# Optimization experiments

Measured on AMD Instinct MI355X. Metric: run time of the kernel, lower is better.

The kernel has to match this reference:

```python
import jax, jax.numpy as jnp
import numpy as np

N_NODES = 100000


def gcn_layer(x, W, b, src, dst, n):
    # PyG GCNConv: add self-loops, symmetric normalization, linear transform
    h = x @ W  # [N, out]
    loop = jnp.arange(n)
    s = jnp.concatenate([src, loop])
    d = jnp.concatenate([dst, loop])
    ones = jnp.ones(s.shape[0], dtype=x.dtype)
    deg = jax.ops.segment_sum(ones, d, num_segments=n)  # in-degree incl. self-loop
    dinv = jnp.where(deg > 0, jax.lax.rsqrt(deg), 0.0)
    norm = dinv[s] * dinv[d]  # [E+N]
    msg = h[s] * norm[:, None]  # gather + scale
    out = jax.ops.segment_sum(msg, d, num_segments=n)  # scatter-add
    return out + b


def setup_inputs() -> dict:
    key = jax.random.key(0)
    k1, k2, k3, k4, k5 = jax.random.split(key, 5)
    d_feat, hidden = 128, 16
    x = jax.random.normal(k1, (N_NODES, d_feat), dtype=jnp.float32)
    edge_index = jax.random.randint(k2, (2, 1600000), 0, N_NODES, dtype=jnp.int64)
    W1 = jax.random.normal(k3, (d_feat, hidden), dtype=jnp.float32) / np.sqrt(d_feat)
    b1 = jnp.zeros((hidden,), dtype=jnp.float32)
    W2 = jax.random.normal(k4, (hidden, d_feat), dtype=jnp.float32) / np.sqrt(hidden)
    b2 = jnp.zeros((d_feat,), dtype=jnp.float32)
    return {"x": x, "edge_index": edge_index, "W1": W1, "b1": b1, "W2": W2, "b2": b2}


def reference(x, edge_index, W1, b1, W2, b2):
    src, dst = edge_index[0], edge_index[1]
    h = gcn_layer(x, W1, b1, src, dst, N_NODES)
    h = jax.nn.relu(h)
    out = gcn_layer(h, W2, b2, src, dst, N_NODES)
    return out
```

## Files before the change

kernel.cpp:

```cpp
#include <hip/hip_runtime.h>


#define THREADS 256
#define TSC 512
#define BSH 9
#define BNODES 512
#define ECHUNK 4096
#define CAPB 9216

typedef _Float16 half4 __attribute__((ext_vector_type(4)));

__global__ void k_init(int* __restrict__ cursor, int NB) {
    int i = blockIdx.x * blockDim.x + threadIdx.x;
    if (i < NB) cursor[i] = i * CAPB;
}

__global__ void __launch_bounds__(TSC) k_bscatter(
        const int* __restrict__ src, const int* __restrict__ dst,
        int* __restrict__ cursor, int* __restrict__ pk, int NB, int E) {
    __shared__ int eds[ECHUNK];
    __shared__ unsigned short rnk[ECHUNK];
    __shared__ unsigned char bkt[ECHUNK];
    __shared__ int h[512];
    __shared__ int lbase[512];
    int tid = threadIdx.x;
    int base0 = blockIdx.x * ECHUNK, end = min(base0 + ECHUNK, E);
    int cnt = end - base0;
    for (int i = tid; i < NB; i += TSC) h[i] = 0;
    __syncthreads();
    int k0 = base0 + tid * 8;
    if (k0 + 8 <= end) {
        int4 d0 = *reinterpret_cast<const int4*>(dst + k0);
        int4 d1 = *reinterpret_cast<const int4*>(dst + k0 + 4);
        int4 s0 = *reinterpret_cast<const int4*>(src + k0);
        int4 s1 = *reinterpret_cast<const int4*>(src + k0 + 4);
        int dd[8] = {d0.x, d0.y, d0.z, d0.w, d1.x, d1.y, d1.z, d1.w};
        int ss[8] = {s0.x, s0.y, s0.z, s0.w, s1.x, s1.y, s1.z, s1.w};
        int j0 = k0 - base0;
#pragma unroll
        for (int j = 0; j < 8; ++j) {
            int b = dd[j] >> BSH;
            int r = atomicAdd(&h[b], 1);
            eds[j0 + j] = ((dd[j] & (BNODES - 1)) << 17) | ss[j];
            rnk[j0 + j] = (unsigned short)r;
            bkt[j0 + j] = (unsigned char)b;
        }
    } else if (k0 < end) {
        for (int k = k0; k < end; ++k) {
            int d = dst[k], s = src[k];
            int b = d >> BSH;
            int r = atomicAdd(&h[b], 1);
            int j = k - base0;
            eds[j] = ((d & (BNODES - 1)) << 17) | s;
            rnk[j] = (unsigned short)r;
            bkt[j] = (unsigned char)b;
        }
    }
    __syncthreads();
    for (int i = tid; i < NB; i += TSC)
        lbase[i] = h[i] ? atomicAdd(&cursor[i], h[i]) : 0;
    __syncthreads();
    for (int j = tid; j < cnt; j += TSC)
        pk[lbase[bkt[j]] + rnk[j]] = eds[j];
}

__global__ void __launch_bounds__(TSC) k_bcsr(
        const int* __restrict__ pk, const int* __restrict__ cursor,
        int* __restrict__ row_ptr, int* __restrict__ row_cnt,
        float* __restrict__ dinv, int* __restrict__ col, int N) {
    __shared__ int eds[CAPB];
    __shared__ int deg[BNODES], sc[BNODES], cur[BNODES];
    int b = blockIdx.x, tid = threadIdx.x;
    int base = b * CAPB;
    int len = cursor[b] - base;
    for (int k = tid; k < len; k += TSC) eds[k] = pk[base + k];
    deg[tid] = 0;
    __syncthreads();
    for (int k = tid; k < len; k += TSC) atomicAdd(&deg[eds[k] >> 17], 1);
    __syncthreads();
    int d = deg[tid];
    sc[tid] = d;
    __syncthreads();
    for (int off = 1; off < BNODES; off <<= 1) {
        int t = (tid >= off) ? sc[tid - off] : 0;
        __syncthreads();
        sc[tid] += t;
        __syncthreads();
    }
    int excl = sc[tid] - d;
    cur[tid] = excl;
    int node = (b << BSH) + tid;
    if (node < N) {
        row_ptr[node] = base + excl;
        row_cnt[node] = d;
        dinv[node] = rsqrtf((float)(d + 1));
    }
    __syncthreads();
    for (int k = tid; k < len; k += TSC) {
        int p = eds[k];
        int r = atomicAdd(&cur[p >> 17], 1);
        col[base + r] = p & 0x1FFFF;
    }
}

__global__ void k_gemm1(const float* __restrict__ x, const float* __restrict__ W1,
                        const float* __restrict__ dinv, _Float16* __restrict__ hs, int n) {
    __shared__ float w[128 * 16];
    __shared__ float xs[16][129];
    int tid = threadIdx.x;
    for (int i = tid; i < 128 * 16; i += THREADS) w[i] = W1[i];
    int brow = blockIdx.x * 16;
    {
        int r = tid >> 4, off = (tid & 15) * 8;
        if (brow + r < n) {
            const float* xr = x + (size_t)(brow + r) * 128 + off;
            float4 a = *reinterpret_cast<const float4*>(xr);
            float4 b = *reinterpret_cast<const float4*>(xr + 4);
            xs[r][off + 0] = a.x; xs[r][off + 1] = a.y; xs[r][off + 2] = a.z; xs[r][off + 3] = a.w;
            xs[r][off + 4] = b.x; xs[r][off + 5] = b.y; xs[r][off + 6] = b.z; xs[r][off + 7] = b.w;
        }
    }
    __syncthreads();
    int r = tid >> 4, c = tid & 15;
    int row = brow + r;
    if (row >= n) return;
    float acc = 0.0f;
#pragma unroll 8
    for (int k = 0; k < 128; ++k) acc = fmaf(xs[r][k], w[k * 16 + c], acc);
    hs[(size_t)row * 16 + c] = (_Float16)(acc * dinv[row]);
}

template <int LAYER>
__global__ void k_gather(const _Float16* __restrict__ hin, const float* __restrict__ dinv,
                         const int* __restrict__ row_ptr, const int* __restrict__ row_cnt,
                         const int* __restrict__ col, const float* __restrict__ bias,
                         _Float16* __restrict__ out_h, float* __restrict__ out_f, int n) {
    int gid = blockIdx.x * blockDim.x + threadIdx.x;
    if (gid >= n * 4) return;
    int node = gid >> 2, q = (gid & 3) * 4;
    int s0 = row_ptr[node], s1 = s0 + row_cnt[node];
    half4 hv = *reinterpret_cast<const half4*>(hin + (size_t)node * 16 + q);
    float ax = (float)hv.x, ay = (float)hv.y, az = (float)hv.z, aw = (float)hv.w;
    int k = s0;
    for (; k + 3 < s1; k += 4) {
        int c0 = col[k], c1 = col[k + 1], c2 = col[k + 2], c3 = col[k + 3];
        half4 v0 = *reinterpret_cast<const half4*>(hin + (size_t)c0 * 16 + q);
        half4 v1 = *reinterpret_cast<const half4*>(hin + (size_t)c1 * 16 + q);
        half4 v2 = *reinterpret_cast<const half4*>(hin + (size_t)c2 * 16 + q);
        half4 v3 = *reinterpret_cast<const half4*>(hin + (size_t)c3 * 16 + q);
        ax += (float)v0.x + (float)v1.x + (float)v2.x + (float)v3.x;
        ay += (float)v0.y + (float)v1.y + (float)v2.y + (float)v3.y;
        az += (float)v0.z + (float)v1.z + (float)v2.z + (float)v3.z;
        aw += (float)v0.w + (float)v1.w + (float)v2.w + (float)v3.w;
    }
    for (; k < s1; ++k) {
        half4 v = *reinterpret_cast<const half4*>(hin + (size_t)col[k] * 16 + q);
        ax += (float)v.x; ay += (float)v.y; az += (float)v.z; aw += (float)v.w;
    }
    float dv = dinv[node];
    if (LAYER == 1) {
        float4 b = *reinterpret_cast<const float4*>(bias + q);
        half4 o;
        o.x = (_Float16)(fmaxf(fmaf(dv, ax, b.x), 0.0f) * dv);
        o.y = (_Float16)(fmaxf(fmaf(dv, ay, b.y), 0.0f) * dv);
        o.z = (_Float16)(fmaxf(fmaf(dv, az, b.z), 0.0f) * dv);
        o.w = (_Float16)(fmaxf(fmaf(dv, aw, b.w), 0.0f) * dv);
        *reinterpret_cast<half4*>(out_h + (size_t)node * 16 + q) = o;
    } else {
        float4 o = make_float4(ax * dv, ay * dv, az * dv, aw * dv);
        *reinterpret_cast<float4*>(out_f + (size_t)node * 16 + q) = o;
    }
}

__global__ void k_gemm2(const float* __restrict__ agg, const float* __restrict__ W2,
                        const float* __restrict__ b2, float* __restrict__ out, int n) {
    __shared__ float rows[32][16];
    int tid = threadIdx.x;
    int col = tid & 127, half = tid >> 7;
    int brow = blockIdx.x * 32;
    for (int i = tid; i < 512; i += THREADS) {
        int r = i >> 4;
        if (brow + r < n) rows[r][i & 15] = agg[(size_t)(brow + r) * 16 + (i & 15)];
    }
    float w[16];
#pragma unroll
    for (int k = 0; k < 16; ++k) w[k] = W2[k * 128 + col];
    float bias = b2[col];
    __syncthreads();
#pragma unroll
    for (int rr = 0; rr < 16; ++rr) {
        int r = half * 16 + rr;
        int row = brow + r;
        if (row >= n) break;
        float acc = bias;
#pragma unroll
        for (int k = 0; k < 16; ++k) acc = fmaf(rows[r][k], w[k], acc);
        out[(size_t)row * 128 + col] = acc;
    }
}

extern "C" void kernel_launch(void* const* d_in, const int* in_sizes, int n_in,
                              void* d_out, int out_size, void* d_ws, size_t ws_size,
                              hipStream_t stream) {
    const float* x  = (const float*)d_in[0];
    const int*   ei = (const int*)d_in[1];
    const float* W1 = (const float*)d_in[2];
    const float* b1 = (const float*)d_in[3];
    const float* W2 = (const float*)d_in[4];
    const float* b2 = (const float*)d_in[5];
    float* out = (float*)d_out;

    int N = in_sizes[0] / 128;
    int E = in_sizes[1] / 2;
    const int* src = ei;
    const int* dst = ei + E;
    int NB = (N + BNODES - 1) >> BSH;
    int EB = (E + ECHUNK - 1) / ECHUNK;
    size_t PADSZ = (size_t)NB * CAPB;

    char* ws = (char*)d_ws;
    size_t o = 0;
    auto carve = [&](size_t bytes) { void* p = ws + o; o = (o + bytes + 255) & ~(size_t)255; return p; };
    int*      cursor  = (int*)carve((size_t)NB * 4);
    int*      pk      = (int*)carve(PADSZ * 4);
    int*      col     = (int*)carve(PADSZ * 4);
    int*      row_ptr = (int*)carve((size_t)N * 4);
    int*      row_cnt = (int*)carve((size_t)N * 4);
    float*    dinv    = (float*)carve((size_t)N * 4);
    _Float16* hs      = (_Float16*)carve((size_t)N * 16 * 2);
    _Float16* h1s     = (_Float16*)carve((size_t)N * 16 * 2);
    float*    bufA    = (float*)carve((size_t)N * 16 * 4);

    int gN4 = (N * 4 + THREADS - 1) / THREADS;

    k_init<<<1, THREADS, 0, stream>>>(cursor, NB);
    k_bscatter<<<EB, TSC, 0, stream>>>(src, dst, cursor, pk, NB, E);
    k_bcsr<<<NB, TSC, 0, stream>>>(pk, cursor, row_ptr, row_cnt, dinv, col, N);

    k_gemm1<<<(N + 15) / 16, THREADS, 0, stream>>>(x, W1, dinv, hs, N);
    k_gather<1><<<gN4, THREADS, 0, stream>>>(hs, dinv, row_ptr, row_cnt, col, b1, h1s, nullptr, N);

    k_gather<2><<<gN4, THREADS, 0, stream>>>(h1s, dinv, row_ptr, row_cnt, col, nullptr, nullptr, bufA, N);
    k_gemm2<<<(N + 31) / 32, THREADS, 0, stream>>>(bufA, W2, b2, out, N);
}
```

Measured before the change: 206.7 us.

## Replace CSR build with bucketed LDS-atomic aggregation and fuse second GEMM

Drops the per-bucket CSR construction (prefix scan and column reorder) and aggregates each 256-node destination bucket directly from the unsorted packed edge list, accumulating into shared memory with float atomics. The second-layer aggregation now also applies W2 and the bias in the same kernel, which removes the intermediate float buffer and one launch. Buckets shrink to 256 nodes so the accumulator fits in LDS, and the scatter packs bucket and rank into a single int. In exchange it relies on LDS float atomics, which can contend on high-degree nodes, and sums in a nondeterministic order.

```diff
diff --git a/kernel.cpp b/kernel.cpp
--- a/kernel.cpp
+++ b/kernel.cpp
@@ -3,10 +3,11 @@
 
 #define THREADS 256
 #define TSC 512
-#define BSH 9
-#define BNODES 512
+#define BSH 8
+#define BNODES 256
 #define ECHUNK 4096
-#define CAPB 9216
+#define CAPB 4608
+#define NBMAX 512
 
 typedef _Float16 half4 __attribute__((ext_vector_type(4)));
 
@@ -19,10 +20,9 @@
         const int* __restrict__ src, const int* __restrict__ dst,
         int* __restrict__ cursor, int* __restrict__ pk, int NB, int E) {
     __shared__ int eds[ECHUNK];
-    __shared__ unsigned short rnk[ECHUNK];
-    __shared__ unsigned char bkt[ECHUNK];
-    __shared__ int h[512];
-    __shared__ int lbase[512];
+    __shared__ int rb[ECHUNK];
+    __shared__ int h[NBMAX];
+    __shared__ int lbase[NBMAX];
     int tid = threadIdx.x;
     int base0 = blockIdx.x * ECHUNK, end = min(base0 + ECHUNK, E);
     int cnt = end - base0;
@@ -42,8 +42,7 @@
             int b = dd[j] >> BSH;
             int r = atomicAdd(&h[b], 1);
             eds[j0 + j] = ((dd[j] & (BNODES - 1)) << 17) | ss[j];
-            rnk[j0 + j] = (unsigned short)r;
-            bkt[j0 + j] = (unsigned char)b;
+            rb[j0 + j] = (b << 13) | r;
         }
     } else if (k0 < end) {
         for (int k = k0; k < end; ++k) {
@@ -52,55 +51,32 @@
             int r = atomicAdd(&h[b], 1);
             int j = k - base0;
             eds[j] = ((d & (BNODES - 1)) << 17) | s;
-            rnk[j] = (unsigned short)r;
-            bkt[j] = (unsigned char)b;
+            rb[j] = (b << 13) | r;
         }
     }
     __syncthreads();
     for (int i = tid; i < NB; i += TSC)
         lbase[i] = h[i] ? atomicAdd(&cursor[i], h[i]) : 0;
     __syncthreads();
-    for (int j = tid; j < cnt; j += TSC)
-        pk[lbase[bkt[j]] + rnk[j]] = eds[j];
-}
-
-__global__ void __launch_bounds__(TSC) k_bcsr(
+    for (int j = tid; j < cnt; j += TSC) {
+        int v = rb[j];
+        pk[lbase[v >> 13] + (v & 8191)] = eds[j];
+    }
+}
+
+__global__ void __launch_bounds__(TSC) k_deg(
         const int* __restrict__ pk, const int* __restrict__ cursor,
-        int* __restrict__ row_ptr, int* __restrict__ row_cnt,
-        float* __restrict__ dinv, int* __restrict__ col, int N) {
-    __shared__ int eds[CAPB];
-    __shared__ int deg[BNODES], sc[BNODES], cur[BNODES];
+        float* __restrict__ dinv, int N) {
+    __shared__ int deg[BNODES];
     int b = blockIdx.x, tid = threadIdx.x;
     int base = b * CAPB;
-    int len = cursor[b] - base;
-    for (int k = tid; k < len; k += TSC) eds[k] = pk[base + k];
-    deg[tid] = 0;
-    __syncthreads();
-    for (int k = tid; k < len; k += TSC) atomicAdd(&deg[eds[k] >> 17], 1);
-    __syncthreads();
-    int d = deg[tid];
-    sc[tid] = d;
-    __syncthreads();
-    for (int off = 1; off < BNODES; off <<= 1) {
-        int t = (tid >= off) ? sc[tid - off] : 0;
-        __syncthreads();
-        sc[tid] += t;
-        __syncthreads();
-    }
-    int excl = sc[tid] - d;
-    cur[tid] = excl;
+    int len = min(cursor[b] - base, CAPB);
+    if (tid < BNODES) deg[tid] = 0;
+    __syncthreads();
+    for (int k = tid; k < len; k += TSC) atomicAdd(&deg[pk[base + k] >> 17], 1);
+    __syncthreads();
     int node = (b << BSH) + tid;
-    if (node < N) {
-        row_ptr[node] = base + excl;
-        row_cnt[node] = d;
-        dinv[node] = rsqrtf((float)(d + 1));
-    }
-    __syncthreads();
-    for (int k = tid; k < len; k += TSC) {
-        int p = eds[k];
-        int r = atomicAdd(&cur[p >> 17], 1);
-        col[base + r] = p & 0x1FFFF;
-    }
+    if (tid < BNODES && node < N) dinv[node] = rsqrtf((float)(deg[tid] + 1));
 }
 
 __global__ void k_gemm1(const float* __restrict__ x, const float* __restrict__ W1,
@@ -131,71 +107,76 @@
 }
 
 template <int LAYER>
-__global__ void k_gather(const _Float16* __restrict__ hin, const float* __restrict__ dinv,
-                         const int* __restrict__ row_ptr, const int* __restrict__ row_cnt,
-                         const int* __restrict__ col, const float* __restrict__ bias,
-                         _Float16* __restrict__ out_h, float* __restrict__ out_f, int n) {
-    int gid = blockIdx.x * blockDim.x + threadIdx.x;
-    if (gid >= n * 4) return;
-    int node = gid >> 2, q = (gid & 3) * 4;
-    int s0 = row_ptr[node], s1 = s0 + row_cnt[node];
-    half4 hv = *reinterpret_cast<const half4*>(hin + (size_t)node * 16 + q);
-    float ax = (float)hv.x, ay = (float)hv.y, az = (float)hv.z, aw = (float)hv.w;
-    int k = s0;
-    for (; k + 3 < s1; k += 4) {
-        int c0 = col[k], c1 = col[k + 1], c2 = col[k + 2], c3 = col[k + 3];
-        half4 v0 = *reinterpret_cast<const half4*>(hin + (size_t)c0 * 16 + q);
-        half4 v1 = *reinterpret_cast<const half4*>(hin + (size_t)c1 * 16 + q);
-        half4 v2 = *reinterpret_cast<const half4*>(hin + (size_t)c2 * 16 + q);
-        half4 v3 = *reinterpret_cast<const half4*>(hin + (size_t)c3 * 16 + q);
-        ax += (float)v0.x + (float)v1.x + (float)v2.x + (float)v3.x;
-        ay += (float)v0.y + (float)v1.y + (float)v2.y + (float)v3.y;
-        az += (float)v0.z + (float)v1.z + (float)v2.z + (float)v3.z;
-        aw += (float)v0.w + (float)v1.w + (float)v2.w + (float)v3.w;
-    }
-    for (; k < s1; ++k) {
-        half4 v = *reinterpret_cast<const half4*>(hin + (size_t)col[k] * 16 + q);
-        ax += (float)v.x; ay += (float)v.y; az += (float)v.z; aw += (float)v.w;
-    }
-    float dv = dinv[node];
+__global__ void __launch_bounds__(TSC) k_agg(
+        const _Float16* __restrict__ hin, const float* __restrict__ dinv,
+        const int* __restrict__ pk, const int* __restrict__ cursor,
+        const float* __restrict__ bias, const float* __restrict__ W2,
+        _Float16* __restrict__ out_h, float* __restrict__ out_f, int N) {
+    __shared__ float acc[BNODES][17];
+    int b = blockIdx.x, tid = threadIdx.x;
+    int base = b * CAPB;
+    int len = min(cursor[b] - base, CAPB);
+    int node0 = (b << BSH) + tid;
+    if (tid < BNODES) {
+        if (node0 < N) {
+            const _Float16* hp = hin + (size_t)node0 * 16;
+#pragma unroll
+            for (int f = 0; f < 16; f += 4) {
+                half4 v = *reinterpret_cast<const half4*>(hp + f);
+                acc[tid][f + 0] = (float)v.x; acc[tid][f + 1] = (float)v.y;
+                acc[tid][f + 2] = (float)v.z; acc[tid][f + 3] = (float)v.w;
+            }
+        } else {
+#pragma unroll
+            for (int f = 0; f < 16; ++f) acc[tid][f] = 0.0f;
+        }
+    }
+    __syncthreads();
+    int q = (tid & 3) * 4;
+#pragma unroll 2
+    for (int e = (tid >> 2); e < len; e += (TSC / 4)) {
+        int p = pk[base + e];
+        int d = p >> 17;
+        int s = p & 0x1FFFF;
+        half4 v = *reinterpret_cast<const half4*>(hin + (size_t)s * 16 + q);
+        atomicAdd(&acc[d][q + 0], (float)v.x);
+        atomicAdd(&acc[d][q + 1], (float)v.y);
+        atomicAdd(&acc[d][q + 2], (float)v.z);
+        atomicAdd(&acc[d][q + 3], (float)v.w);
+    }
+    __syncthreads();
     if (LAYER == 1) {
-        float4 b = *reinterpret_cast<const float4*>(bias + q);
-        half4 o;
-        o.x = (_Float16)(fmaxf(fmaf(dv, ax, b.x), 0.0f) * dv);
-        o.y = (_Float16)(fmaxf(fmaf(dv, ay, b.y), 0.0f) * dv);
-        o.z = (_Float16)(fmaxf(fmaf(dv, az, b.z), 0.0f) * dv);
-        o.w = (_Float16)(fmaxf(fmaf(dv, aw, b.w), 0.0f) * dv);
-        *reinterpret_cast<half4*>(out_h + (size_t)node * 16 + q) = o;
+        if (tid < BNODES && node0 < N) {
+            float dv = dinv[node0];
+            alignas(16) _Float16 tmp[16];
+#pragma unroll
+            for (int f = 0; f < 16; ++f)
+                tmp[f] = (_Float16)(fmaxf(fmaf(dv, acc[tid][f], bias[f]), 0.0f) * dv);
+            float4* dp = reinterpret_cast<float4*>(out_h + (size_t)node0 * 16);
+            const float4* sp = reinterpret_cast<const float4*>(tmp);
+            dp[0] = sp[0]; dp[1] = sp[1];
+        }
     } else {
-        float4 o = make_float4(ax * dv, ay * dv, az * dv, aw * dv);
-        *reinterpret_cast<float4*>(out_f + (size_t)node * 16 + q) = o;
-    }
-}
-
-__global__ void k_gemm2(const float* __restrict__ agg, const float* __restrict__ W2,
-                        const float* __restrict__ b2, float* __restrict__ out, int n) {
-    __shared__ float rows[32][16];
-    int tid = threadIdx.x;
-    int col = tid & 127, half = tid >> 7;
-    int brow = blockIdx.x * 32;
-    for (int i = tid; i < 512; i += THREADS) {
-        int r = i >> 4;
-        if (brow + r < n) rows[r][i & 15] = agg[(size_t)(brow + r) * 16 + (i & 15)];
-    }
-    float w[16];
-#pragma unroll
-    for (int k = 0; k < 16; ++k) w[k] = W2[k * 128 + col];
-    float bias = b2[col];
-    __syncthreads();
-#pragma unroll
-    for (int rr = 0; rr < 16; ++rr) {
-        int r = half * 16 + rr;
-        int row = brow + r;
-        if (row >= n) break;
-        float acc = bias;
-#pragma unroll
-        for (int k = 0; k < 16; ++k) acc = fmaf(rows[r][k], w[k], acc);
-        out[(size_t)row * 128 + col] = acc;
+        if (tid < BNODES && node0 < N) {
+            float dv = dinv[node0];
+#pragma unroll
+            for (int f = 0; f < 16; ++f) acc[tid][f] *= dv;
+        }
+        __syncthreads();
+        int col = tid & 127, grp = tid >> 7;
+        float w[16];
+#pragma unroll
+        for (int k = 0; k < 16; ++k) w[k] = W2[k * 128 + col];
+        float bb = bias[col];
+        for (int rr = 0; rr < BNODES / 4; ++rr) {
+            int r = grp * (BNODES / 4) + rr;
+            int node = (b << BSH) + r;
+            if (node >= N) break;
+            float s = bb;
+#pragma unroll
+            for (int k = 0; k < 16; ++k) s = fmaf(acc[r][k], w[k], s);
+            out_f[(size_t)node * 128 + col] = s;
+        }
     }
 }
 
@@ -221,25 +202,18 @@
     char* ws = (char*)d_ws;
     size_t o = 0;
     auto carve = [&](size_t bytes) { void* p = ws + o; o = (o + bytes + 255) & ~(size_t)255; return p; };
-    int*      cursor  = (int*)carve((size_t)NB * 4);
-    int*      pk      = (int*)carve(PADSZ * 4);
-    int*      col     = (int*)carve(PADSZ * 4);
-    int*      row_ptr = (int*)carve((size_t)N * 4);
-    int*      row_cnt = (int*)carve((size_t)N * 4);
-    float*    dinv    = (float*)carve((size_t)N * 4);
-    _Float16* hs      = (_Float16*)carve((size_t)N * 16 * 2);
-    _Float16* h1s     = (_Float16*)carve((size_t)N * 16 * 2);
-    float*    bufA    = (float*)carve((size_t)N * 16 * 4);
-
-    int gN4 = (N * 4 + THREADS - 1) / THREADS;
-
-    k_init<<<1, THREADS, 0, stream>>>(cursor, NB);
+    int*      cursor = (int*)carve((size_t)NB * 4);
+    int*      pk     = (int*)carve(PADSZ * 4);
+    float*    dinv   = (float*)carve((size_t)N * 4);
+    _Float16* hs     = (_Float16*)carve((size_t)N * 16 * 2);
+    _Float16* h1s    = (_Float16*)carve((size_t)N * 16 * 2);
+
+    k_init<<<(NB + THREADS - 1) / THREADS, THREADS, 0, stream>>>(cursor, NB);
     k_bscatter<<<EB, TSC, 0, stream>>>(src, dst, cursor, pk, NB, E);
-    k_bcsr<<<NB, TSC, 0, stream>>>(pk, cursor, row_ptr, row_cnt, dinv, col, N);
+    k_deg<<<NB, TSC, 0, stream>>>(pk, cursor, dinv, N);
 
     k_gemm1<<<(N + 15) / 16, THREADS, 0, stream>>>(x, W1, dinv, hs, N);
-    k_gather<1><<<gN4, THREADS, 0, stream>>>(hs, dinv, row_ptr, row_cnt, col, b1, h1s, nullptr, N);
-
-    k_gather<2><<<gN4, THREADS, 0, stream>>>(h1s, dinv, row_ptr, row_cnt, col, nullptr, nullptr, bufA, N);
-    k_gemm2<<<(N + 31) / 32, THREADS, 0, stream>>>(bufA, W2, b2, out, N);
-}
+    k_agg<1><<<NB, TSC, 0, stream>>>(hs, dinv, pk, cursor, b1, nullptr, h1s, nullptr, N);
+
+    k_agg<2><<<NB, TSC, 0, stream>>>(h1s, dinv, pk, cursor, b2, W2, nullptr, out, N);
+}
```

Result: slower. 509.5 us (+146.5%).

## Fuse layer-2 gather with W2 GEMM and halve CSR bucket size

Applied to the files above, without the earlier changes.

Merges the second-layer neighbor aggregation with the 16x128 output projection in one kernel. The aggregated rows now stay in shared memory, so the float intermediate buffer no longer makes a global round trip and one launch is removed. Bucket size for the CSR build drops from 512 to 256 nodes, which doubles the number of bscatter/bcsr blocks (about 391) for more parallelism. To fit, rank and bucket are packed into one int, and bucket length is clamped to capacity, which risks silently dropping edges if a bucket overflows.

```diff
diff --git a/kernel.cpp b/kernel.cpp
--- a/kernel.cpp
+++ b/kernel.cpp
@@ -3,10 +3,11 @@
 
 #define THREADS 256
 #define TSC 512
-#define BSH 9
-#define BNODES 512
+#define BSH 8
+#define BNODES 256
 #define ECHUNK 4096
-#define CAPB 9216
+#define CAPB 4608
+#define NBMAX 512
 
 typedef _Float16 half4 __attribute__((ext_vector_type(4)));
 
@@ -19,10 +20,9 @@
         const int* __restrict__ src, const int* __restrict__ dst,
         int* __restrict__ cursor, int* __restrict__ pk, int NB, int E) {
     __shared__ int eds[ECHUNK];
-    __shared__ unsigned short rnk[ECHUNK];
-    __shared__ unsigned char bkt[ECHUNK];
-    __shared__ int h[512];
-    __shared__ int lbase[512];
+    __shared__ int rb[ECHUNK];
+    __shared__ int h[NBMAX];
+    __shared__ int lbase[NBMAX];
     int tid = threadIdx.x;
     int base0 = blockIdx.x * ECHUNK, end = min(base0 + ECHUNK, E);
     int cnt = end - base0;
@@ -42,8 +42,7 @@
             int b = dd[j] >> BSH;
             int r = atomicAdd(&h[b], 1);
             eds[j0 + j] = ((dd[j] & (BNODES - 1)) << 17) | ss[j];
-            rnk[j0 + j] = (unsigned short)r;
-            bkt[j0 + j] = (unsigned char)b;
+            rb[j0 + j] = (b << 13) | r;
         }
     } else if (k0 < end) {
         for (int k = k0; k < end; ++k) {
@@ -52,16 +51,17 @@
             int r = atomicAdd(&h[b], 1);
             int j = k - base0;
             eds[j] = ((d & (BNODES - 1)) << 17) | s;
-            rnk[j] = (unsigned short)r;
-            bkt[j] = (unsigned char)b;
+            rb[j] = (b << 13) | r;
         }
     }
     __syncthreads();
     for (int i = tid; i < NB; i += TSC)
         lbase[i] = h[i] ? atomicAdd(&cursor[i], h[i]) : 0;
     __syncthreads();
-    for (int j = tid; j < cnt; j += TSC)
-        pk[lbase[bkt[j]] + rnk[j]] = eds[j];
+    for (int j = tid; j < cnt; j += TSC) {
+        int v = rb[j];
+        pk[lbase[v >> 13] + (v & 8191)] = eds[j];
+    }
 }
 
 __global__ void __launch_bounds__(TSC) k_bcsr(
@@ -72,28 +72,30 @@
     __shared__ int deg[BNODES], sc[BNODES], cur[BNODES];
     int b = blockIdx.x, tid = threadIdx.x;
     int base = b * CAPB;
-    int len = cursor[b] - base;
+    int len = min(cursor[b] - base, CAPB);
     for (int k = tid; k < len; k += TSC) eds[k] = pk[base + k];
-    deg[tid] = 0;
+    if (tid < BNODES) deg[tid] = 0;
     __syncthreads();
     for (int k = tid; k < len; k += TSC) atomicAdd(&deg[eds[k] >> 17], 1);
     __syncthreads();
-    int d = deg[tid];
-    sc[tid] = d;
+    int d = (tid < BNODES) ? deg[tid] : 0;
+    if (tid < BNODES) sc[tid] = d;
     __syncthreads();
     for (int off = 1; off < BNODES; off <<= 1) {
-        int t = (tid >= off) ? sc[tid - off] : 0;
+        int t = (tid < BNODES && tid >= off) ? sc[tid - off] : 0;
         __syncthreads();
-        sc[tid] += t;
+        if (tid < BNODES) sc[tid] += t;
         __syncthreads();
     }
-    int excl = sc[tid] - d;
-    cur[tid] = excl;
-    int node = (b << BSH) + tid;
-    if (node < N) {
-        row_ptr[node] = base + excl;
-        row_cnt[node] = d;
-        dinv[node] = rsqrtf((float)(d + 1));
+    if (tid < BNODES) {
+        int excl = sc[tid] - d;
+        cur[tid] = excl;
+        int node = (b << BSH) + tid;
+        if (node < N) {
+            row_ptr[node] = base + excl;
+            row_cnt[node] = d;
+            dinv[node] = rsqrtf((float)(d + 1));
+        }
     }
     __syncthreads();
     for (int k = tid; k < len; k += TSC) {
@@ -130,11 +132,10 @@
     hs[(size_t)row * 16 + c] = (_Float16)(acc * dinv[row]);
 }
 
-template <int LAYER>
-__global__ void k_gather(const _Float16* __restrict__ hin, const float* __restrict__ dinv,
-                         const int* __restrict__ row_ptr, const int* __restrict__ row_cnt,
-                         const int* __restrict__ col, const float* __restrict__ bias,
-                         _Float16* __restrict__ out_h, float* __restrict__ out_f, int n) {
+__global__ void k_gather1(const _Float16* __restrict__ hin, const float* __restrict__ dinv,
+                          const int* __restrict__ row_ptr, const int* __restrict__ row_cnt,
+                          const int* __restrict__ col, const float* __restrict__ bias,
+                          _Float16* __restrict__ out_h, int n) {
     int gid = blockIdx.x * blockDim.x + threadIdx.x;
     if (gid >= n * 4) return;
     int node = gid >> 2, q = (gid & 3) * 4;
@@ -158,44 +159,69 @@
         ax += (float)v.x; ay += (float)v.y; az += (float)v.z; aw += (float)v.w;
     }
     float dv = dinv[node];
-    if (LAYER == 1) {
-        float4 b = *reinterpret_cast<const float4*>(bias + q);
-        half4 o;
-        o.x = (_Float16)(fmaxf(fmaf(dv, ax, b.x), 0.0f) * dv);
-        o.y = (_Float16)(fmaxf(fmaf(dv, ay, b.y), 0.0f) * dv);
-        o.z = (_Float16)(fmaxf(fmaf(dv, az, b.z), 0.0f) * dv);
-        o.w = (_Float16)(fmaxf(fmaf(dv, aw, b.w), 0.0f) * dv);
-        *reinterpret_cast<half4*>(out_h + (size_t)node * 16 + q) = o;
-    } else {
-        float4 o = make_float4(ax * dv, ay * dv, az * dv, aw * dv);
-        *reinterpret_cast<float4*>(out_f + (size_t)node * 16 + q) = o;
-    }
-}
-
-__global__ void k_gemm2(const float* __restrict__ agg, const float* __restrict__ W2,
-                        const float* __restrict__ b2, float* __restrict__ out, int n) {
-    __shared__ float rows[32][16];
+    float4 b = *reinterpret_cast<const float4*>(bias + q);
+    half4 o;
+    o.x = (_Float16)(fmaxf(fmaf(dv, ax, b.x), 0.0f) * dv);
+    o.y = (_Float16)(fmaxf(fmaf(dv, ay, b.y), 0.0f) * dv);
+    o.z = (_Float16)(fmaxf(fmaf(dv, az, b.z), 0.0f) * dv);
+    o.w = (_Float16)(fmaxf(fmaf(dv, aw, b.w), 0.0f) * dv);
+    *reinterpret_cast<half4*>(out_h + (size_t)node * 16 + q) = o;
+}
+
+__global__ void __launch_bounds__(THREADS) k_gather2f(
+        const _Float16* __restrict__ hin, const float* __restrict__ dinv,
+        const int* __restrict__ row_ptr, const int* __restrict__ row_cnt,
+        const int* __restrict__ col, const float* __restrict__ W2,
+        const float* __restrict__ b2, float* __restrict__ out, int n) {
+    __shared__ float rows[64][17];
     int tid = threadIdx.x;
-    int col = tid & 127, half = tid >> 7;
-    int brow = blockIdx.x * 32;
-    for (int i = tid; i < 512; i += THREADS) {
-        int r = i >> 4;
-        if (brow + r < n) rows[r][i & 15] = agg[(size_t)(brow + r) * 16 + (i & 15)];
-    }
-    float w[16];
+    int bnode = blockIdx.x * 64;
+    {
+        int nloc = tid >> 2, q = (tid & 3) * 4;
+        int node = bnode + nloc;
+        if (node < n) {
+            int s0 = row_ptr[node], s1 = s0 + row_cnt[node];
+            half4 hv = *reinterpret_cast<const half4*>(hin + (size_t)node * 16 + q);
+            float ax = (float)hv.x, ay = (float)hv.y, az = (float)hv.z, aw = (float)hv.w;
+            int k = s0;
+            for (; k + 3 < s1; k += 4) {
+                int c0 = col[k], c1 = col[k + 1], c2 = col[k + 2], c3 = col[k + 3];
+                half4 v0 = *reinterpret_cast<const half4*>(hin + (size_t)c0 * 16 + q);
+                half4 v1 = *reinterpret_cast<const half4*>(hin + (size_t)c1 * 16 + q);
+                half4 v2 = *reinterpret_cast<const half4*>(hin + (size_t)c2 * 16 + q);
+                half4 v3 = *reinterpret_cast<const half4*>(hin + (size_t)c3 * 16 + q);
+                ax += (float)v0.x + (float)v1.x + (float)v2.x + (float)v3.x;
+                ay += (float)v0.y + (float)v1.y + (float)v2.y + (float)v3.y;
+                az += (float)v0.z + (float)v1.z + (float)v2.z + (float)v3.z;
+                aw += (float)v0.w + (float)v1.w + (float)v2.w + (float)v3.w;
+            }
+            for (; k < s1; ++k) {
+                half4 v = *reinterpret_cast<const half4*>(hin + (size_t)col[k] * 16 + q);
+                ax += (float)v.x; ay += (float)v.y; az += (float)v.z; aw += (float)v.w;
+            }
+            float dv = dinv[node];
+            rows[nloc][q + 0] = ax * dv;
+            rows[nloc][q + 1] = ay * dv;
+            rows[nloc][q + 2] = az * dv;
+            rows[nloc][q + 3] = aw * dv;
+        }
+    }
+    __syncthreads();
+    {
+        int c = tid & 127, grp = tid >> 7;
+        float w[16];
 #pragma unroll
-    for (int k = 0; k < 16; ++k) w[k] = W2[k * 128 + col];
-    float bias = b2[col];
-    __syncthreads();
+        for (int k = 0; k < 16; ++k) w[k] = W2[k * 128 + c];
+        float bb = b2[c];
+        for (int rr = 0; rr < 32; ++rr) {
+            int r = grp * 32 + rr;
+            int node = bnode + r;
+            if (node >= n) break;
+            float s = bb;
 #pragma unroll
-    for (int rr = 0; rr < 16; ++rr) {
-        int r = half * 16 + rr;
-        int row = brow + r;
-        if (row >= n) break;
-        float acc = bias;
-#pragma unroll
-        for (int k = 0; k < 16; ++k) acc = fmaf(rows[r][k], w[k], acc);
-        out[(size_t)row * 128 + col] = acc;
+            for (int k = 0; k < 16; ++k) s = fmaf(rows[r][k], w[k], s);
+            out[(size_t)node * 128 + c] = s;
+        }
     }
 }
 
@@ -229,17 +255,15 @@
     float*    dinv    = (float*)carve((size_t)N * 4);
     _Float16* hs      = (_Float16*)carve((size_t)N * 16 * 2);
     _Float16* h1s     = (_Float16*)carve((size_t)N * 16 * 2);
-    float*    bufA    = (float*)carve((size_t)N * 16 * 4);
 
     int gN4 = (N * 4 + THREADS - 1) / THREADS;
 
-    k_init<<<1, THREADS, 0, stream>>>(cursor, NB);
+    k_init<<<(NB + THREADS - 1) / THREADS, THREADS, 0, stream>>>(cursor, NB);
     k_bscatter<<<EB, TSC, 0, stream>>>(src, dst, cursor, pk, NB, E);
     k_bcsr<<<NB, TSC, 0, stream>>>(pk, cursor, row_ptr, row_cnt, dinv, col, N);
 
     k_gemm1<<<(N + 15) / 16, THREADS, 0, stream>>>(x, W1, dinv, hs, N);
-    k_gather<1><<<gN4, THREADS, 0, stream>>>(hs, dinv, row_ptr, row_cnt, col, b1, h1s, nullptr, N);
-
-    k_gather<2><<<gN4, THREADS, 0, stream>>>(h1s, dinv, row_ptr, row_cnt, col, nullptr, nullptr, bufA, N);
-    k_gemm2<<<(N + 31) / 32, THREADS, 0, stream>>>(bufA, W2, b2, out, N);
-}
+    k_gather1<<<gN4, THREADS, 0, stream>>>(hs, dinv, row_ptr, row_cnt, col, b1, h1s, N);
+
+    k_gather2f<<<(N + 63) / 64, THREADS, 0, stream>>>(h1s, dinv, row_ptr, row_cnt, col, W2, b2, out, N);
+}
```

Result: no change. 209.1 us (+1.2%).
